# Performance work log

Measured on AMD Instinct MI355X. Metric: run time of the kernel, lower is better.

The kernel has to match this reference:

```python
import jax, jax.numpy as jnp
import numpy as np

ORIENTATIONS = 8
CELL = 16          # pixels_per_cell = (16, 16)
EPS = 1e-5         # skimage L2-Hys eps


def _hog_features(x):
    """x: [B, H, W, C] float image. Faithful to skimage.feature.hog with
    orientations=8, pixels_per_cell=(16,16), cells_per_block=(1,1),
    block_norm='L2-Hys', multichannel gradient selection."""
    B, H, W, C = x.shape
    # per-channel central-difference gradients, zero at borders (skimage _hog_channel_gradient)
    g_row = jnp.zeros_like(x).at[:, 1:-1, :, :].set(x[:, 2:, :, :] - x[:, :-2, :, :])
    g_col = jnp.zeros_like(x).at[:, :, 1:-1, :].set(x[:, :, 2:, :] - x[:, :, :-2, :])
    magn_ch = jnp.hypot(g_row, g_col)                      # [B,H,W,C]
    # pick channel with max gradient magnitude per pixel
    idx = jnp.argmax(magn_ch, axis=-1, keepdims=True)      # [B,H,W,1]
    gr = jnp.take_along_axis(g_row, idx, axis=-1)[..., 0]  # [B,H,W]
    gc = jnp.take_along_axis(g_col, idx, axis=-1)[..., 0]
    magn = jnp.take_along_axis(magn_ch, idx, axis=-1)[..., 0]
    # orientation in degrees, mod 180 (unsigned gradients)
    ori = jnp.degrees(jnp.arctan2(gr, gc)) % 180.0
    bin_width = 180.0 / ORIENTATIONS
    bin_idx = jnp.clip(jnp.floor(ori / bin_width).astype(jnp.int32), 0, ORIENTATIONS - 1)
    ncr, ncc = H // CELL, W // CELL
    # per-cell mean magnitude for each orientation bin
    hists = []
    for o in range(ORIENTATIONS):
        m = jnp.where(bin_idx == o, magn, 0.0)             # [B,H,W]
        m = m.reshape(B, ncr, CELL, ncc, CELL).mean(axis=(2, 4))  # [B,ncr,ncc]
        hists.append(m)
    hist = jnp.stack(hists, axis=-1)                       # [B,ncr,ncc,O]
    # block normalization: 1x1 cells per block, 'L2-Hys'
    n = hist / jnp.sqrt(jnp.sum(hist * hist, axis=-1, keepdims=True) + EPS ** 2)
    n = jnp.minimum(n, 0.2)
    n = n / jnp.sqrt(jnp.sum(n * n, axis=-1, keepdims=True) + EPS ** 2)
    return n.reshape(B, -1)                                # [B, ncr*ncc*O]


def setup_inputs() -> dict:
    key = jax.random.key(0)
    fake = jax.random.uniform(key, (64, 3, 512, 512), dtype=jnp.float32)
    return {"fake": fake}


def reference(fake) -> jnp.ndarray:
    x = jnp.transpose(fake, (0, 2, 3, 1))  # NCHW -> NHWC (module's permute)
    return _hog_features(x)
```

## Files before the change

kernel.cpp:

```cpp
#include <hip/hip_runtime.h>
#include <math.h>


namespace {

constexpr int Hh = 512;
constexpr int Ww = 512;
constexpr int CH = 3;

__global__ __launch_bounds__(256) void hog_kernel(const float* __restrict__ x,
                                                  float* __restrict__ out) {
    const int bx = blockIdx.x;
    const int cg = bx & 7;
    const int cr = (bx >> 3) & 31;
    const int b  = bx >> 8;
    const int tx = threadIdx.x;
    const int wl = tx & 63;
    const int rg = tx >> 6;
    const int w  = cg * 64 + wl;
    const int cell = wl >> 4;

    float hist[8];
#pragma unroll
    for (int o = 0; o < 8; ++o) hist[o] = 0.f;

    const float* xb = x + (size_t)b * (CH * Hh * Ww);

#pragma unroll
    for (int it = 0; it < 4; ++it) {
        const int h = cr * 16 + rg + it * 4;

        float best_m = -1.f, best_gr = 0.f, best_gc = 0.f;
#pragma unroll
        for (int c = 0; c < CH; ++c) {
            const float* p = xb + (c * Hh + h) * Ww + w;
            float xu = 0.f, xd = 0.f;
            if (h > 0 && h < Hh - 1) { xu = p[-Ww]; xd = p[Ww]; }
            float xl = 0.f, xr = 0.f;
            if (w > 0 && w < Ww - 1) { xl = p[-1]; xr = p[1]; }
            const float grow = xd - xu;
            const float gcol = xr - xl;
            const float m = sqrtf(grow * grow + gcol * gcol);
            if (m > best_m) { best_m = m; best_gr = grow; best_gc = gcol; }
        }

        float ang = atan2f(best_gr, best_gc) * 57.29577951308232f;
        float ori = fmodf(ang, 180.0f);
        if (ori < 0.f) ori += 180.0f;
        int bin = (int)floorf(ori / 22.5f);
        bin = bin < 0 ? 0 : (bin > 7 ? 7 : bin);

#pragma unroll
        for (int o = 0; o < 8; ++o) hist[o] += (bin == o) ? best_m : 0.f;
    }

#pragma unroll
    for (int mask = 1; mask < 16; mask <<= 1) {
#pragma unroll
        for (int o = 0; o < 8; ++o) hist[o] += __shfl_xor(hist[o], mask, 64);
    }

    __shared__ float lhist[4][4][8];
    if ((wl & 15) == 0) {
#pragma unroll
        for (int o = 0; o < 8; ++o) lhist[rg][cell][o] = hist[o];
    }
    __syncthreads();

    if (tx < 32) {
        const int c4 = tx >> 3, o = tx & 7;
        float hv = (lhist[0][c4][o] + lhist[1][c4][o] +
                    lhist[2][c4][o] + lhist[3][c4][o]) * (1.0f / 256.0f);

        float ss = hv * hv;
#pragma unroll
        for (int mask = 1; mask < 8; mask <<= 1) ss += __shfl_xor(ss, mask, 64);
        float n1 = hv / sqrtf(ss + 1e-10f);
        n1 = fminf(n1, 0.2f);
        float ss2 = n1 * n1;
#pragma unroll
        for (int mask = 1; mask < 8; mask <<= 1) ss2 += __shfl_xor(ss2, mask, 64);
        const float nv = n1 / sqrtf(ss2 + 1e-10f);

        const size_t oi = (((size_t)b * 32 + cr) * 32 + (cg * 4 + c4)) * 8 + o;
        out[oi] = nv;
    }
}

}

extern "C" void kernel_launch(void* const* d_in, const int* in_sizes, int n_in,
                              void* d_out, int out_size, void* d_ws, size_t ws_size,
                              hipStream_t stream) {
    (void)n_in; (void)out_size; (void)d_ws; (void)ws_size;
    const float* x = (const float*)d_in[0];
    float* out = (float*)d_out;
    const int B = in_sizes[0] / (CH * Hh * Ww);
    const int grid = B * 32 * 8;
    hog_kernel<<<grid, 256, 0, stream>>>(x, out);
}
```

Baseline: 307.9 us.

## Use sliding row window with float4 loads and atan-free cumulative orientation binning

Each thread now handles 8 contiguous pixels loaded as float4 pairs and keeps a rolling three-row register window, so vertical neighbours are reused instead of reloaded. Horizontal neighbours at the ends come from lane shuffles. The atan2, fmod and floor binning is replaced by tan(22.5°) threshold comparisons that build cumulative bin sums, which are differenced at the end. The grid shrinks to 16 blocks per image, each covering a 32-row band. This raises register pressure and gives fewer blocks, and boundary-tie binning may differ slightly from atan2.

```diff
diff --git a/kernel.cpp b/kernel.cpp
--- a/kernel.cpp
+++ b/kernel.cpp
@@ -6,83 +6,140 @@
 
 constexpr int Hh = 512;
 constexpr int Ww = 512;
-constexpr int CH = 3;
+constexpr int CHN = 3;
+constexpr int HW = Hh * Ww;
+constexpr float TAN22 = 0.41421356237309503f;
+
+__device__ __forceinline__ void load_row(const float* __restrict__ xb,
+                                         int h, int lane, float dst[CHN][8]) {
+    const int hl = h < 0 ? 0 : (h > Hh - 1 ? Hh - 1 : h);
+#pragma unroll
+    for (int ch = 0; ch < CHN; ++ch) {
+        const float4* p =
+            (const float4*)(xb + (size_t)ch * HW + (size_t)hl * Ww) + (lane << 1);
+        const float4 a = p[0];
+        const float4 b = p[1];
+        dst[ch][0] = a.x; dst[ch][1] = a.y; dst[ch][2] = a.z; dst[ch][3] = a.w;
+        dst[ch][4] = b.x; dst[ch][5] = b.y; dst[ch][6] = b.z; dst[ch][7] = b.w;
+    }
+}
 
 __global__ __launch_bounds__(256) void hog_kernel(const float* __restrict__ x,
                                                   float* __restrict__ out) {
-    const int bx = blockIdx.x;
-    const int cg = bx & 7;
-    const int cr = (bx >> 3) & 31;
-    const int b  = bx >> 8;
-    const int tx = threadIdx.x;
-    const int wl = tx & 63;
-    const int rg = tx >> 6;
-    const int w  = cg * 64 + wl;
-    const int cell = wl >> 4;
+    const int b     = blockIdx.x >> 4;
+    const int band2 = blockIdx.x & 15;
+    const int tx    = threadIdx.x;
+    const int lane  = tx & 63;
+    const int rg    = tx >> 6;
+    const int r0    = band2 * 32 + rg * 8;
+    const bool isL0  = (lane == 0);
+    const bool isL63 = (lane == 63);
 
-    float hist[8];
+    const float* xb = x + (size_t)b * (CHN * HW);
+
+    float c[8];
 #pragma unroll
-    for (int o = 0; o < 8; ++o) hist[o] = 0.f;
+    for (int o = 0; o < 8; ++o) c[o] = 0.f;
 
-    const float* xb = x + (size_t)b * (CH * Hh * Ww);
+    float win[3][CHN][8];
+    load_row(xb, r0 - 1, lane, win[0]);
+    load_row(xb, r0,     lane, win[1]);
+    load_row(xb, r0 + 1, lane, win[2]);
 
 #pragma unroll
-    for (int it = 0; it < 4; ++it) {
-        const int h = cr * 16 + rg + it * 4;
+    for (int hh = 0; hh < 8; ++hh) {
+        const int h = r0 + hh;
+        float (*prev)[8] = win[hh % 3];
+        float (*cur)[8]  = win[(hh + 1) % 3];
+        float (*next)[8] = win[(hh + 2) % 3];
+        const bool rowEdge = (h == 0) | (h == Hh - 1);
 
-        float best_m = -1.f, best_gr = 0.f, best_gc = 0.f;
+        float grow[CHN][8];
 #pragma unroll
-        for (int c = 0; c < CH; ++c) {
-            const float* p = xb + (c * Hh + h) * Ww + w;
-            float xu = 0.f, xd = 0.f;
-            if (h > 0 && h < Hh - 1) { xu = p[-Ww]; xd = p[Ww]; }
-            float xl = 0.f, xr = 0.f;
-            if (w > 0 && w < Ww - 1) { xl = p[-1]; xr = p[1]; }
-            const float grow = xd - xu;
-            const float gcol = xr - xl;
-            const float m = sqrtf(grow * grow + gcol * gcol);
-            if (m > best_m) { best_m = m; best_gr = grow; best_gc = gcol; }
+        for (int ch = 0; ch < CHN; ++ch)
+#pragma unroll
+            for (int i = 0; i < 8; ++i)
+                grow[ch][i] = rowEdge ? 0.f : next[ch][i] - prev[ch][i];
+
+        if (hh < 7) load_row(xb, h + 2, lane, win[hh % 3]);
+
+        float shL[CHN], shR[CHN];
+#pragma unroll
+        for (int ch = 0; ch < CHN; ++ch) {
+            shL[ch] = __shfl_up(cur[ch][7], 1, 64);
+            shR[ch] = __shfl_down(cur[ch][0], 1, 64);
         }
 
-        float ang = atan2f(best_gr, best_gc) * 57.29577951308232f;
-        float ori = fmodf(ang, 180.0f);
-        if (ori < 0.f) ori += 180.0f;
-        int bin = (int)floorf(ori / 22.5f);
-        bin = bin < 0 ? 0 : (bin > 7 ? 7 : bin);
+#pragma unroll
+        for (int i = 0; i < 8; ++i) {
+            float bm2 = -1.f, bgr = 0.f, bgc = 0.f;
+#pragma unroll
+            for (int ch = 0; ch < CHN; ++ch) {
+                const float gl = (i == 0) ? shL[ch] : cur[ch][i - 1];
+                const float gr_ = (i == 7) ? shR[ch] : cur[ch][i + 1];
+                float gcol = gr_ - gl;
+                if (i == 0) gcol = isL0 ? 0.f : gcol;
+                if (i == 7) gcol = isL63 ? 0.f : gcol;
+                const float gv = grow[ch][i];
+                const float m2 = fmaf(gv, gv, gcol * gcol);
+                if (m2 > bm2) { bm2 = m2; bgr = gv; bgc = gcol; }
+            }
+            const float m = sqrtf(bm2);
 
-#pragma unroll
-        for (int o = 0; o < 8; ++o) hist[o] += (bin == o) ? best_m : 0.f;
+            const bool flip = (bgr < 0.f) | ((bgr == 0.f) & (bgc < 0.f));
+            const float bb = flip ? -bgr : bgr;
+            const float A  = flip ? -bgc : bgc;
+            const float Aa = fabsf(A);
+            const float p1 = Aa * TAN22;
+            const float p2 = bb * TAN22;
+            const bool q2  = (A <= 0.f);
+            const bool ge1 = (bb >= p1), ge2 = (bb >= Aa), ge3 = (p2 >= Aa);
+            const bool gt1 = (bb > p1),  gt2 = (bb > Aa),  gt3 = (p2 > Aa);
+            c[0] += m;
+            c[1] += (q2 | ge1) ? m : 0.f;
+            c[2] += (q2 | ge2) ? m : 0.f;
+            c[3] += (q2 | ge3) ? m : 0.f;
+            c[4] += q2 ? m : 0.f;
+            c[5] += (q2 & !gt3) ? m : 0.f;
+            c[6] += (q2 & !gt2) ? m : 0.f;
+            c[7] += (q2 & !gt1) ? m : 0.f;
+        }
     }
 
 #pragma unroll
-    for (int mask = 1; mask < 16; mask <<= 1) {
+    for (int o = 0; o < 8; ++o) c[o] += __shfl_xor(c[o], 1, 64);
+
+    __shared__ float lhist[4][32][9];
+    if (tx < 128) lhist[tx >> 5][tx & 31][8] = 0.f;
+    if ((lane & 1) == 0) {
+        const int cellc = lane >> 1;
 #pragma unroll
-        for (int o = 0; o < 8; ++o) hist[o] += __shfl_xor(hist[o], mask, 64);
-    }
-
-    __shared__ float lhist[4][4][8];
-    if ((wl & 15) == 0) {
-#pragma unroll
-        for (int o = 0; o < 8; ++o) lhist[rg][cell][o] = hist[o];
+        for (int o = 0; o < 8; ++o) lhist[rg][cellc][o] = c[o];
     }
     __syncthreads();
 
-    if (tx < 32) {
-        const int c4 = tx >> 3, o = tx & 7;
-        float hv = (lhist[0][c4][o] + lhist[1][c4][o] +
-                    lhist[2][c4][o] + lhist[3][c4][o]) * (1.0f / 256.0f);
+    const int cell = tx >> 3;
+    const int o    = tx & 7;
+#pragma unroll
+    for (int band = 0; band < 2; ++band) {
+        const float c_o  = lhist[2 * band][cell][o]     + lhist[2 * band + 1][cell][o];
+        const float c_o1 = lhist[2 * band][cell][o + 1] + lhist[2 * band + 1][cell][o + 1];
+        const float hv = (c_o - c_o1) * (1.0f / 256.0f);
 
         float ss = hv * hv;
-#pragma unroll
-        for (int mask = 1; mask < 8; mask <<= 1) ss += __shfl_xor(ss, mask, 64);
+        ss += __shfl_xor(ss, 1, 64);
+        ss += __shfl_xor(ss, 2, 64);
+        ss += __shfl_xor(ss, 4, 64);
         float n1 = hv / sqrtf(ss + 1e-10f);
         n1 = fminf(n1, 0.2f);
-        float ss2 = n1 * n1;
-#pragma unroll
-        for (int mask = 1; mask < 8; mask <<= 1) ss2 += __shfl_xor(ss2, mask, 64);
-        const float nv = n1 / sqrtf(ss2 + 1e-10f);
+        float s2 = n1 * n1;
+        s2 += __shfl_xor(s2, 1, 64);
+        s2 += __shfl_xor(s2, 2, 64);
+        s2 += __shfl_xor(s2, 4, 64);
+        const float nv = n1 / sqrtf(s2 + 1e-10f);
 
-        const size_t oi = (((size_t)b * 32 + cr) * 32 + (cg * 4 + c4)) * 8 + o;
+        const size_t oi =
+            (((size_t)b * 32 + (band2 * 2 + band)) * 32 + cell) * 8 + o;
         out[oi] = nv;
     }
 }
@@ -95,7 +152,7 @@
     (void)n_in; (void)out_size; (void)d_ws; (void)ws_size;
     const float* x = (const float*)d_in[0];
     float* out = (float*)d_out;
-    const int B = in_sizes[0] / (CH * Hh * Ww);
-    const int grid = B * 32 * 8;
+    const int B = in_sizes[0] / (CHN * HW);
+    const int grid = B * 16;
     hog_kernel<<<grid, 256, 0, stream>>>(x, out);
 }
```

Measured after the change: 281.5 us. 8.6% less time.
